# Optimization experiments

Hardware: AMD Instinct MI355X
Metric: run time of the kernel (lower is better)

Reference implementation:

```python
import jax, jax.numpy as jnp
import numpy as np

N, E, XD = 100000, 300000, 32
H, C = 4, 64          # heads, per-head out channels
D = H * C             # 256, node feature width
L = 3                 # num_message_passing
EPS = 1e-5
NEG_SLOPE = 0.2


def setup_inputs() -> dict:
    key = jax.random.key(0)
    ks = jax.random.split(key, 16)
    s = 0.05
    return {
        "x": jax.random.normal(ks[0], (N, XD), jnp.float32),
        "edge_index": jax.random.randint(ks[1], (2, E), 0, N, jnp.int32),
        "edge_type": jax.random.randint(ks[2], (E,), 0, 3, jnp.int32),
        "edge_feat": jax.random.uniform(ks[3], (E,), jnp.float32),
        # pre-encoder Linear(x_dim -> D)
        "W0": jax.random.normal(ks[4], (XD, D), jnp.float32) * s,
        "b0": jnp.zeros((D,), jnp.float32),
        # per-layer GATv2 params, stacked over L layers
        "Wl": jax.random.normal(ks[5], (L, D, D), jnp.float32) * s,
        "bl": jnp.zeros((L, D), jnp.float32),
        "Wr": jax.random.normal(ks[6], (L, D, D), jnp.float32) * s,
        "br": jnp.zeros((L, D), jnp.float32),
        "We": jax.random.normal(ks[7], (L, 4, D), jnp.float32) * s,  # lin_edge (no bias)
        "att": jax.random.normal(ks[8], (L, H, C), jnp.float32) * s,
        "bo": jnp.zeros((L, D), jnp.float32),
        # graph-mode LayerNorm (single module, reused every layer)
        "gamma": jnp.ones((D,), jnp.float32),
        "beta": jnp.zeros((D,), jnp.float32),
    }


def _graph_layernorm(h, gamma, beta):
    # PyG LayerNorm(mode='graph'): normalize over ALL nodes and features of the graph
    mu = jnp.mean(h)
    hc = h - mu
    var = jnp.mean(hc * hc)
    return hc * jax.lax.rsqrt(var + EPS) * gamma + beta


def _gatv2_layer(h, src, dst, eattr, Wl, bl, Wr, br, We, att, bo):
    xl = (h @ Wl + bl).reshape(N, H, C)
    xr = (h @ Wr + br).reshape(N, H, C)
    ea = (eattr @ We).reshape(E, H, C)
    e = jax.nn.leaky_relu(xl[src] + xr[dst] + ea, NEG_SLOPE)   # [E,H,C]
    alpha = jnp.einsum('ehc,hc->eh', e, att)                    # [E,H]
    amax = jax.ops.segment_max(alpha, dst, num_segments=N)     # [N,H]
    ex = jnp.exp(alpha - amax[dst])
    denom = jax.ops.segment_sum(ex, dst, num_segments=N)       # [N,H]
    a = ex / denom[dst]                                         # softmax per dst node
    msg = xl[src] * a[:, :, None]                               # [E,H,C]
    out = jax.ops.segment_sum(msg, dst, num_segments=N)        # [N,H,C]
    return out.reshape(N, D) + bo


def reference(x, edge_index, edge_type, edge_feat,
              W0, b0, Wl, bl, Wr, br, We, att, bo, gamma, beta):
    # edge feature construction: one-hot(type over 3) ++ scalar feature (== torch cat/where path)
    eattr = jnp.concatenate(
        [jax.nn.one_hot(edge_type, 3, dtype=x.dtype), edge_feat[:, None]], axis=-1)  # [E,4]
    src, dst = edge_index[0], edge_index[1]   # messages flow src -> dst
    h = jax.nn.relu(x @ W0 + b0)              # pre_enc (dropout = identity in eval)
    for i in range(L):
        g = _gatv2_layer(h, src, dst, eattr, Wl[i], bl[i], Wr[i], br[i], We[i], att[i], bo[i])
        h = _graph_layernorm(jax.nn.relu(g), gamma, beta)
    return h
```

## Files before the change

### kernel.cpp

```cpp
#include <hip/hip_runtime.h>
#include <hip/hip_bf16.h>

#define NN 100000
#define EE 300000
#define DD 256
#define HH 4
#define CC 64
#define LL 3
#define SCAN_CHUNK 1024

#define MPAD 100096

typedef __attribute__((ext_vector_type(8))) short bh8;
typedef __attribute__((ext_vector_type(4))) float f32x4;

__device__ inline float bf2f(unsigned short u) {
    union { float f; unsigned int i; } c; c.i = ((unsigned int)u) << 16; return c.f;
}
__device__ inline unsigned short f2bf(float x) {
    __hip_bfloat16 b = __float2bfloat16(x);
    return *reinterpret_cast<unsigned short*>(&b);
}


__global__ __launch_bounds__(256) void k_count(const int* __restrict__ dst, int* __restrict__ deg, int E_) {
    int e = blockIdx.x * 256 + threadIdx.x;
    if (e < E_) atomicAdd(&deg[dst[e]], 1);
}

__global__ __launch_bounds__(256) void k_scan1(const int* __restrict__ deg, int* __restrict__ bsum, int n) {
    int b = blockIdx.x;
    int base = b * SCAN_CHUNK;
    int t = threadIdx.x;
    int s = 0;
    for (int i = t; i < SCAN_CHUNK; i += 256) {
        int idx = base + i;
        if (idx < n) s += deg[idx];
    }
    __shared__ int sdata[256];
    sdata[t] = s;
    __syncthreads();
    for (int off = 128; off > 0; off >>= 1) {
        if (t < off) sdata[t] += sdata[t + off];
        __syncthreads();
    }
    if (t == 0) bsum[b] = sdata[0];
}

__global__ void k_scan2(const int* __restrict__ bsum, int* __restrict__ boff, int nb,
                        int* __restrict__ offsets, int n) {
    if (threadIdx.x == 0 && blockIdx.x == 0) {
        int run = 0;
        for (int i = 0; i < nb; i++) { boff[i] = run; run += bsum[i]; }
        offsets[n] = run;
    }
}

__global__ __launch_bounds__(256) void k_scan3(const int* __restrict__ deg, const int* __restrict__ boff,
                                               int* __restrict__ offsets, int n) {
    int b = blockIdx.x, t = threadIdx.x;
    int base = b * SCAN_CHUNK;
    int i0 = base + t * 4;
    int v[4]; int sum = 0;
    #pragma unroll
    for (int j = 0; j < 4; j++) {
        int idx = i0 + j;
        v[j] = (idx < n) ? deg[idx] : 0;
        sum += v[j];
    }
    __shared__ int sdata[256];
    sdata[t] = sum;
    __syncthreads();
    for (int off = 1; off < 256; off <<= 1) {
        int x = (t >= off) ? sdata[t - off] : 0;
        __syncthreads();
        sdata[t] += x;
        __syncthreads();
    }
    int excl = (t == 0) ? 0 : sdata[t - 1];
    int run = boff[b] + excl;
    #pragma unroll
    for (int j = 0; j < 4; j++) {
        int idx = i0 + j;
        if (idx < n) offsets[idx] = run;
        run += v[j];
    }
}

__global__ __launch_bounds__(256) void k_fill(const int* __restrict__ src, const int* __restrict__ dst,
                                              const int* __restrict__ ety, const float* __restrict__ efe,
                                              const int* __restrict__ offsets, int* __restrict__ cursor,
                                              int* __restrict__ csr_src, float* __restrict__ csr_feat, int E_) {
    int e = blockIdx.x * 256 + threadIdx.x;
    if (e < E_) {
        int d = dst[e];
        int pos = offsets[d] + atomicAdd(&cursor[d], 1);
        csr_src[pos] = src[e] | (ety[e] << 24);
        csr_feat[pos] = efe[e];
    }
}

__global__ __launch_bounds__(256) void k_cvtw(const float* __restrict__ Wl, const float* __restrict__ Wr,
                                              unsigned short* __restrict__ Wct) {
    int mat = blockIdx.z;
    int layer = mat >> 1, which = mat & 1;
    const float* src = (which ? Wr : Wl) + (size_t)layer * DD * DD;
    unsigned short* dst = Wct + (size_t)layer * 512 * DD + (size_t)which * DD * DD;
    int k0 = blockIdx.x * 64, n0 = blockIdx.y * 64;
    __shared__ float tile[64][65];
    int tx = threadIdx.x & 63, ty = threadIdx.x >> 6;
    #pragma unroll
    for (int i = 0; i < 16; i++) {
        int r = i * 4 + ty;
        tile[r][tx] = src[(size_t)(k0 + r) * DD + n0 + tx];
    }
    __syncthreads();
    #pragma unroll
    for (int i = 0; i < 16; i++) {
        int r = i * 4 + ty;
        dst[(size_t)(n0 + r) * DD + k0 + tx] = f2bf(tile[tx][r]);
    }
}

__global__ __launch_bounds__(256) void k_bias(const float* __restrict__ bl, const float* __restrict__ br,
                                              float* __restrict__ bc) {
    int i = blockIdx.x * 256 + threadIdx.x;
    if (i < LL * 512) {
        int l = i >> 9, j = i & 511;
        bc[i] = (j < 256) ? bl[l * DD + j] : br[l * DD + j - 256];
    }
}

__global__ __launch_bounds__(256) void k_preenc(const float* __restrict__ x, const float* __restrict__ W0,
                                                const float* __restrict__ b0, unsigned short* __restrict__ act) {
    __shared__ float xs[8][32];
    int t = threadIdx.x;
    int nb = blockIdx.x * 8;
    {
        int m = t >> 5, k = t & 31;
        xs[m][k] = x[(size_t)(nb + m) * 32 + k];
    }
    __syncthreads();
    float acc[8];
    float b = b0[t];
    #pragma unroll
    for (int m = 0; m < 8; m++) acc[m] = b;
    for (int k = 0; k < 32; k++) {
        float w = W0[k * DD + t];
        #pragma unroll
        for (int m = 0; m < 8; m++) acc[m] += xs[m][k] * w;
    }
    #pragma unroll
    for (int m = 0; m < 8; m++) {
        act[(size_t)(nb + m) * DD + t] = f2bf(fmaxf(acc[m], 0.f));
    }
}

__global__ __launch_bounds__(256, 3) void k_gemm(const unsigned short* __restrict__ act,
                                                 const unsigned short* __restrict__ Wct,
                                                 const float* __restrict__ bc,
                                                 unsigned short* __restrict__ xlr) {
    __shared__ short As[128][136];
    int t = threadIdx.x;
    int lane = t & 63;
    int w = t >> 6;
    int wm = w >> 1, wn = w & 1;
    size_t rowBase = (size_t)blockIdx.x * 128;
    int n0 = blockIdx.y * 128;
    int rsel = lane & 15, kq = lane >> 4;

    const unsigned short* Bw = Wct + (size_t)(n0 + wn * 64) * DD;

    f32x4 acc[4][4];
    #pragma unroll
    for (int i = 0; i < 4; i++)
        #pragma unroll
        for (int j = 0; j < 4; j++)
            acc[i][j] = (f32x4){0.f, 0.f, 0.f, 0.f};

    #pragma unroll
    for (int j = 0; j < 8; j++) {
        int idx = t + j * 256;
        int row = idx >> 4, c = idx & 15;
        *(bh8*)&As[row][c * 8] = *(const bh8*)(act + (rowBase + row) * DD + c * 8);
    }

    bh8 bcur[4], bnxt[4];
    #pragma unroll
    for (int ni = 0; ni < 4; ni++)
        bcur[ni] = *(const bh8*)(Bw + (size_t)(ni * 16 + rsel) * DD + kq * 8);

    __syncthreads();

    #pragma unroll
    for (int s = 0; s < 8; ++s) {
        if (s == 4) {
            __syncthreads();
            #pragma unroll
            for (int j = 0; j < 8; j++) {
                int idx = t + j * 256;
                int row = idx >> 4, c = idx & 15;
                *(bh8*)&As[row][c * 8] = *(const bh8*)(act + (rowBase + row) * DD + 128 + c * 8);
            }
            __syncthreads();
        }
        if (s < 7) {
            int s2 = s + 1;
            int kb2 = (s2 >> 2) * 128 + (s2 & 3) * 32 + kq * 8;
            #pragma unroll
            for (int ni = 0; ni < 4; ni++)
                bnxt[ni] = *(const bh8*)(Bw + (size_t)(ni * 16 + rsel) * DD + kb2);
        }
        int ksel = (s & 3) * 32 + kq * 8;
        bh8 af[4];
        #pragma unroll
        for (int mi = 0; mi < 4; mi++)
            af[mi] = *(const bh8*)&As[wm * 64 + mi * 16 + rsel][ksel];
        #pragma unroll
        for (int mi = 0; mi < 4; mi++)
            #pragma unroll
            for (int ni = 0; ni < 4; ni++)
                acc[mi][ni] = __builtin_amdgcn_mfma_f32_16x16x32_bf16(af[mi], bcur[ni], acc[mi][ni], 0, 0, 0);
        #pragma unroll
        for (int ni = 0; ni < 4; ni++) bcur[ni] = bnxt[ni];
    }

    __syncthreads();
    short* stage = &As[0][0];
    #pragma unroll
    for (int ni = 0; ni < 4; ni++) {
        int col = wn * 64 + ni * 16 + rsel;
        float bias = bc[n0 + col];
        #pragma unroll
        for (int mi = 0; mi < 4; mi++) {
            int r0 = wm * 64 + mi * 16 + kq * 4;
            #pragma unroll
            for (int j = 0; j < 4; j++)
                stage[(r0 + j) * 136 + col] = (short)f2bf(acc[mi][ni][j] + bias);
        }
    }
    __syncthreads();
    #pragma unroll
    for (int j = 0; j < 8; j++) {
        int idx = t + j * 256;
        int row = idx >> 4, c = idx & 15;
        size_t grow = rowBase + row;
        if (grow < NN)
            *(bh8*)(xlr + grow * 512 + n0 + c * 8) = *(const bh8*)&stage[row * 136 + c * 8];
    }
}

__global__ __launch_bounds__(256) void k_aggregate(const unsigned short* __restrict__ xlr,
                                                   const int* __restrict__ offsets,
                                                   const int* __restrict__ csr_src, const float* __restrict__ csr_feat,
                                                   const float* __restrict__ We, const float* __restrict__ att,
                                                   const float* __restrict__ bo,
                                                   unsigned short* __restrict__ act, float2* __restrict__ partial) {
    int lane = threadIdx.x & 63;
    int n = blockIdx.x * 4 + (threadIdx.x >> 6);
    int c0 = lane * 4;

    float4 attv = *(const float4*)(att + c0);
    float4 we3 = *(const float4*)(We + 3 * DD + c0);
    float4 w0v = *(const float4*)(We + 0 * DD + c0);
    float4 w1v = *(const float4*)(We + 1 * DD + c0);
    float4 w2v = *(const float4*)(We + 2 * DD + c0);

    uint2 xrr = *(const uint2*)(xlr + (size_t)n * 512 + 256 + c0);
    float xr0 = bf2f((unsigned short)(xrr.x & 0xffff));
    float xr1 = bf2f((unsigned short)(xrr.x >> 16));
    float xr2 = bf2f((unsigned short)(xrr.y & 0xffff));
    float xr3 = bf2f((unsigned short)(xrr.y >> 16));

    float b00 = xr0 + w0v.x, b01 = xr1 + w0v.y, b02 = xr2 + w0v.z, b03 = xr3 + w0v.w;
    float b10 = xr0 + w1v.x, b11 = xr1 + w1v.y, b12 = xr2 + w1v.z, b13 = xr3 + w1v.w;
    float b20 = xr0 + w2v.x, b21 = xr1 + w2v.y, b22 = xr2 + w2v.z, b23 = xr3 + w2v.w;

    int start = offsets[n], end = offsets[n + 1];
    float s = 0.f, a0 = 0.f, a1 = 0.f, a2 = 0.f, a3 = 0.f;
    int i = start;
    for (; i + 2 <= end; i += 2) {
        int pA = csr_src[i];     float fA = csr_feat[i];
        int pB = csr_src[i + 1]; float fB = csr_feat[i + 1];
        uint2 xvA = *(const uint2*)(xlr + (size_t)(pA & 0xFFFFF) * 512 + c0);
        uint2 xvB = *(const uint2*)(xlr + (size_t)(pB & 0xFFFFF) * 512 + c0);
        int tyA = pA >> 24, tyB = pB >> 24;
        float xA0 = bf2f((unsigned short)(xvA.x & 0xffff));
        float xA1 = bf2f((unsigned short)(xvA.x >> 16));
        float xA2 = bf2f((unsigned short)(xvA.y & 0xffff));
        float xA3 = bf2f((unsigned short)(xvA.y >> 16));
        float xB0 = bf2f((unsigned short)(xvB.x & 0xffff));
        float xB1 = bf2f((unsigned short)(xvB.x >> 16));
        float xB2 = bf2f((unsigned short)(xvB.y & 0xffff));
        float xB3 = bf2f((unsigned short)(xvB.y >> 16));
        float sA0 = (tyA == 0) ? b00 : (tyA == 1) ? b10 : b20;
        float sA1 = (tyA == 0) ? b01 : (tyA == 1) ? b11 : b21;
        float sA2 = (tyA == 0) ? b02 : (tyA == 1) ? b12 : b22;
        float sA3 = (tyA == 0) ? b03 : (tyA == 1) ? b13 : b23;
        float sB0 = (tyB == 0) ? b00 : (tyB == 1) ? b10 : b20;
        float sB1 = (tyB == 0) ? b01 : (tyB == 1) ? b11 : b21;
        float sB2 = (tyB == 0) ? b02 : (tyB == 1) ? b12 : b22;
        float sB3 = (tyB == 0) ? b03 : (tyB == 1) ? b13 : b23;
        float eA0 = xA0 + fmaf(fA, we3.x, sA0); eA0 = fmaxf(eA0, 0.2f * eA0);
        float eA1 = xA1 + fmaf(fA, we3.y, sA1); eA1 = fmaxf(eA1, 0.2f * eA1);
        float eA2 = xA2 + fmaf(fA, we3.z, sA2); eA2 = fmaxf(eA2, 0.2f * eA2);
        float eA3 = xA3 + fmaf(fA, we3.w, sA3); eA3 = fmaxf(eA3, 0.2f * eA3);
        float eB0 = xB0 + fmaf(fB, we3.x, sB0); eB0 = fmaxf(eB0, 0.2f * eB0);
        float eB1 = xB1 + fmaf(fB, we3.y, sB1); eB1 = fmaxf(eB1, 0.2f * eB1);
        float eB2 = xB2 + fmaf(fB, we3.z, sB2); eB2 = fmaxf(eB2, 0.2f * eB2);
        float eB3 = xB3 + fmaf(fB, we3.w, sB3); eB3 = fmaxf(eB3, 0.2f * eB3);
        float dA = attv.x * eA0 + attv.y * eA1 + attv.z * eA2 + attv.w * eA3;
        float dB = attv.x * eB0 + attv.y * eB1 + attv.z * eB2 + attv.w * eB3;
        dA += __shfl_xor(dA, 1, 64);  dB += __shfl_xor(dB, 1, 64);
        dA += __shfl_xor(dA, 2, 64);  dB += __shfl_xor(dB, 2, 64);
        dA += __shfl_xor(dA, 4, 64);  dB += __shfl_xor(dB, 4, 64);
        dA += __shfl_xor(dA, 8, 64);  dB += __shfl_xor(dB, 8, 64);
        float pa = __expf(fminf(fmaxf(dA, -60.f), 60.f));
        float pb = __expf(fminf(fmaxf(dB, -60.f), 60.f));
        s += pa + pb;
        a0 = fmaf(pa, xA0, fmaf(pb, xB0, a0));
        a1 = fmaf(pa, xA1, fmaf(pb, xB1, a1));
        a2 = fmaf(pa, xA2, fmaf(pb, xB2, a2));
        a3 = fmaf(pa, xA3, fmaf(pb, xB3, a3));
    }
    if (i < end) {
        int pA = csr_src[i]; float fA = csr_feat[i];
        uint2 xvA = *(const uint2*)(xlr + (size_t)(pA & 0xFFFFF) * 512 + c0);
        int tyA = pA >> 24;
        float xA0 = bf2f((unsigned short)(xvA.x & 0xffff));
        float xA1 = bf2f((unsigned short)(xvA.x >> 16));
        float xA2 = bf2f((unsigned short)(xvA.y & 0xffff));
        float xA3 = bf2f((unsigned short)(xvA.y >> 16));
        float sA0 = (tyA == 0) ? b00 : (tyA == 1) ? b10 : b20;
        float sA1 = (tyA == 0) ? b01 : (tyA == 1) ? b11 : b21;
        float sA2 = (tyA == 0) ? b02 : (tyA == 1) ? b12 : b22;
        float sA3 = (tyA == 0) ? b03 : (tyA == 1) ? b13 : b23;
        float eA0 = xA0 + fmaf(fA, we3.x, sA0); eA0 = fmaxf(eA0, 0.2f * eA0);
        float eA1 = xA1 + fmaf(fA, we3.y, sA1); eA1 = fmaxf(eA1, 0.2f * eA1);
        float eA2 = xA2 + fmaf(fA, we3.z, sA2); eA2 = fmaxf(eA2, 0.2f * eA2);
        float eA3 = xA3 + fmaf(fA, we3.w, sA3); eA3 = fmaxf(eA3, 0.2f * eA3);
        float dA = attv.x * eA0 + attv.y * eA1 + attv.z * eA2 + attv.w * eA3;
        dA += __shfl_xor(dA, 1, 64);
        dA += __shfl_xor(dA, 2, 64);
        dA += __shfl_xor(dA, 4, 64);
        dA += __shfl_xor(dA, 8, 64);
        float pa = __expf(fminf(fmaxf(dA, -60.f), 60.f));
        s += pa;
        a0 = fmaf(pa, xA0, a0);
        a1 = fmaf(pa, xA1, a1);
        a2 = fmaf(pa, xA2, a2);
        a3 = fmaf(pa, xA3, a3);
    }
    float inv = (end > start) ? __builtin_amdgcn_rcpf(s) : 0.f;
    float4 bov = *(const float4*)(bo + c0);
    float o0 = fmaxf(fmaf(a0, inv, bov.x), 0.f);
    float o1 = fmaxf(fmaf(a1, inv, bov.y), 0.f);
    float o2 = fmaxf(fmaf(a2, inv, bov.z), 0.f);
    float o3 = fmaxf(fmaf(a3, inv, bov.w), 0.f);
    uint2 pk;
    pk.x = (unsigned int)f2bf(o0) | ((unsigned int)f2bf(o1) << 16);
    pk.y = (unsigned int)f2bf(o2) | ((unsigned int)f2bf(o3) << 16);
    *(uint2*)(act + (size_t)n * DD + c0) = pk;

    float v1 = o0 + o1 + o2 + o3;
    float v2 = o0 * o0 + o1 * o1 + o2 * o2 + o3 * o3;
    #pragma unroll
    for (int off = 32; off > 0; off >>= 1) {
        v1 += __shfl_xor(v1, off, 64);
        v2 += __shfl_xor(v2, off, 64);
    }
    if (lane == 0) partial[n] = make_float2(v1, v2);
}

__global__ __launch_bounds__(256) void k_lnreduce(const float2* __restrict__ partial,
                                                  double2* __restrict__ partial2) {
    int b = blockIdx.x, t = threadIdx.x;
    double s1 = 0.0, s2 = 0.0;
    for (int i = b * 256 + t; i < NN; i += 64 * 256) {
        float2 p = partial[i];
        s1 += p.x; s2 += p.y;
    }
    __shared__ double d1[256], d2[256];
    d1[t] = s1; d2[t] = s2;
    __syncthreads();
    for (int off = 128; off > 0; off >>= 1) {
        if (t < off) { d1[t] += d1[t + off]; d2[t] += d2[t + off]; }
        __syncthreads();
    }
    if (t == 0) partial2[b] = (double2){d1[0], d2[0]};
}

__global__ __launch_bounds__(256) void k_stats(const double2* __restrict__ partial2,
                                               const float* __restrict__ gamma, const float* __restrict__ beta,
                                               float* __restrict__ sc, float* __restrict__ vsh) {
    __shared__ double d1[64], d2[64];
    int t = threadIdx.x;
    if (t < 64) { double2 p = partial2[t]; d1[t] = p.x; d2[t] = p.y; }
    __syncthreads();
    for (int off = 32; off > 0; off >>= 1) {
        if (t < off) { d1[t] += d1[t + off]; d2[t] += d2[t + off]; }
        __syncthreads();
    }
    const double M = (double)NN * DD;
    double mu = d1[0] / M;
    double var = d2[0] / M - mu * mu;
    float rs = rsqrtf((float)(var + 1e-5));
    float scv = rs * gamma[t];
    sc[t] = scv;
    vsh[t] = beta[t] - (float)mu * scv;
}

__global__ __launch_bounds__(256) void k_foldw(const unsigned short* __restrict__ Wct,
                                               const float* __restrict__ bcL,
                                               const float* __restrict__ sc, const float* __restrict__ vsh,
                                               unsigned short* __restrict__ Wct2, float* __restrict__ bc2) {
    int row = (blockIdx.x << 2) + (threadIdx.x >> 6);
    int lane = threadIdx.x & 63;
    int k0 = lane * 4;
    uint2 raw = *(const uint2*)(Wct + (size_t)row * DD + k0);
    float w0 = bf2f((unsigned short)(raw.x & 0xffff));
    float w1 = bf2f((unsigned short)(raw.x >> 16));
    float w2 = bf2f((unsigned short)(raw.y & 0xffff));
    float w3 = bf2f((unsigned short)(raw.y >> 16));
    float4 scv = *(const float4*)(sc + k0);
    float4 vv  = *(const float4*)(vsh + k0);
    uint2 pk;
    pk.x = (unsigned int)f2bf(w0 * scv.x) | ((unsigned int)f2bf(w1 * scv.y) << 16);
    pk.y = (unsigned int)f2bf(w2 * scv.z) | ((unsigned int)f2bf(w3 * scv.w) << 16);
    *(uint2*)(Wct2 + (size_t)row * DD + k0) = pk;
    float d = w0 * vv.x + w1 * vv.y + w2 * vv.z + w3 * vv.w;
    #pragma unroll
    for (int off = 32; off > 0; off >>= 1) d += __shfl_xor(d, off, 64);
    if (lane == 0) bc2[row] = bcL[row] + d;
}

__global__ __launch_bounds__(256) void k_final(const unsigned short* __restrict__ act,
                                               const float* __restrict__ sc, const float* __restrict__ vsh,
                                               float* __restrict__ h) {
    size_t i = ((size_t)blockIdx.x * 256 + threadIdx.x) * 4;
    uint2 raw = *(const uint2*)(act + i);
    int ch = (int)(i & (DD - 1));
    float4 scv = *(const float4*)(sc + ch);
    float4 vv  = *(const float4*)(vsh + ch);
    float4 o;
    o.x = fmaf(bf2f((unsigned short)(raw.x & 0xffff)), scv.x, vv.x);
    o.y = fmaf(bf2f((unsigned short)(raw.x >> 16)),    scv.y, vv.y);
    o.z = fmaf(bf2f((unsigned short)(raw.y & 0xffff)), scv.z, vv.z);
    o.w = fmaf(bf2f((unsigned short)(raw.y >> 16)),    scv.w, vv.w);
    *reinterpret_cast<float4*>(h + i) = o;
}


extern "C" void kernel_launch(void* const* d_in, const int* in_sizes, int n_in,
                              void* d_out, int out_size, void* d_ws, size_t ws_size,
                              hipStream_t stream) {
    const float* x    = (const float*)d_in[0];
    const int*   ei   = (const int*)d_in[1];
    const int*   ety  = (const int*)d_in[2];
    const float* efe  = (const float*)d_in[3];
    const float* W0   = (const float*)d_in[4];
    const float* b0   = (const float*)d_in[5];
    const float* Wl   = (const float*)d_in[6];
    const float* bl   = (const float*)d_in[7];
    const float* Wr   = (const float*)d_in[8];
    const float* br   = (const float*)d_in[9];
    const float* We   = (const float*)d_in[10];
    const float* att  = (const float*)d_in[11];
    const float* bo   = (const float*)d_in[12];
    const float* gamma= (const float*)d_in[13];
    const float* beta = (const float*)d_in[14];
    float* h = (float*)d_out;

    char* base = (char*)d_ws;
    size_t off = 0;
    auto carve = [&](size_t bytes) -> void* {
        void* p = base + off;
        off += (bytes + 255) & ~(size_t)255;
        return p;
    };
    unsigned short* act  = (unsigned short*)carve((size_t)MPAD * DD * 2);
    unsigned short* xlr  = (unsigned short*)carve((size_t)NN * 512 * 2);
    unsigned short* Wct  = (unsigned short*)carve((size_t)LL * 512 * DD * 2);
    unsigned short* Wct2 = (unsigned short*)carve((size_t)512 * DD * 2);
    float* bc            = (float*)carve((size_t)LL * 512 * 4);
    float* bc2           = (float*)carve((size_t)512 * 4);
    float* sc            = (float*)carve((size_t)DD * 4);
    float* vsh           = (float*)carve((size_t)DD * 4);
    int*   deg      = (int*)carve((size_t)NN * 4);
    int*   offsets  = (int*)carve((size_t)(NN + 1) * 4);
    int*   bsum     = (int*)carve(1024);
    int*   boff     = (int*)carve(1024);
    int*   csr_src  = (int*)carve((size_t)EE * 4);
    float* csr_feat = (float*)carve((size_t)EE * 4);
    float2* partial = (float2*)carve((size_t)NN * 8);
    double2* partial2 = (double2*)carve((size_t)64 * 16);

    const int NB = (NN + SCAN_CHUNK - 1) / SCAN_CHUNK;

    hipMemsetAsync(deg, 0, (size_t)NN * 4, stream);
    k_count<<<(EE + 255) / 256, 256, 0, stream>>>(ei + EE, deg, EE);
    k_scan1<<<NB, 256, 0, stream>>>(deg, bsum, NN);
    k_scan2<<<1, 64, 0, stream>>>(bsum, boff, NB, offsets, NN);
    k_scan3<<<NB, 256, 0, stream>>>(deg, boff, offsets, NN);
    hipMemsetAsync(deg, 0, (size_t)NN * 4, stream);
    k_fill<<<(EE + 255) / 256, 256, 0, stream>>>(ei, ei + EE, ety, efe, offsets, deg,
                                                 csr_src, csr_feat, EE);

    k_cvtw<<<dim3(4, 4, 6), 256, 0, stream>>>(Wl, Wr, Wct);
    k_bias<<<6, 256, 0, stream>>>(bl, br, bc);

    k_preenc<<<NN / 8, 256, 0, stream>>>(x, W0, b0, act);

    for (int l = 0; l < LL; l++) {
        const unsigned short* Wg = (l == 0) ? Wct : Wct2;
        const float* bg = (l == 0) ? bc : bc2;
        k_gemm<<<dim3(MPAD / 128, 4), 256, 0, stream>>>(act, Wg, bg, xlr);
        k_aggregate<<<NN / 4, 256, 0, stream>>>(xlr, offsets, csr_src, csr_feat,
                                                We + (size_t)l * 4 * DD, att + (size_t)l * HH * CC,
                                                bo + (size_t)l * DD, act, partial);
        k_lnreduce<<<64, 256, 0, stream>>>(partial, partial2);
        k_stats<<<1, 256, 0, stream>>>(partial2, gamma, beta, sc, vsh);
        if (l < LL - 1)
            k_foldw<<<128, 256, 0, stream>>>(Wct + (size_t)(l + 1) * 512 * DD, bc + (size_t)(l + 1) * 512,
                                             sc, vsh, Wct2, bc2);
    }
    k_final<<<(NN * DD / 4) / 256, 256, 0, stream>>>(act, sc, vsh, h);
}
```

Measured before the change: 542.0 us.

## Retile GEMM to 64-row blocks covering all 512 output columns

The GEMM block now loads a 64-row activation tile with the full K=256 into LDS once, and uses 8 waves that each compute 64 output columns, so one block covers all 512 columns. Previously a 2D grid used 128x128 tiles, which reloaded each activation row four times and refilled LDS midway through K. The output is staged in two halves through LDS. This removes redundant activation reads, but each wave now streams its own weight slice, and occupancy changes with the 512-thread blocks and the larger LDS footprint.

```diff
diff --git a/kernel.cpp b/kernel.cpp
--- a/kernel.cpp
+++ b/kernel.cpp
@@ -156,20 +156,25 @@
     }
 }
 
-__global__ __launch_bounds__(256, 3) void k_gemm(const unsigned short* __restrict__ act,
-                                                 const unsigned short* __restrict__ Wct,
-                                                 const float* __restrict__ bc,
-                                                 unsigned short* __restrict__ xlr) {
-    __shared__ short As[128][136];
+__global__ __launch_bounds__(512) void k_gemm(const unsigned short* __restrict__ act,
+                                              const unsigned short* __restrict__ Wct,
+                                              const float* __restrict__ bc,
+                                              unsigned short* __restrict__ xlr) {
+    __shared__ short lds[16896];
     int t = threadIdx.x;
     int lane = t & 63;
     int w = t >> 6;
-    int wm = w >> 1, wn = w & 1;
-    size_t rowBase = (size_t)blockIdx.x * 128;
-    int n0 = blockIdx.y * 128;
+    size_t rowBase = (size_t)blockIdx.x * 64;
     int rsel = lane & 15, kq = lane >> 4;
 
-    const unsigned short* Bw = Wct + (size_t)(n0 + wn * 64) * DD;
+    #pragma unroll
+    for (int j = 0; j < 4; j++) {
+        int idx = t + j * 512;
+        int row = idx >> 5, c = idx & 31;
+        *(bh8*)&lds[row * 260 + c * 8] = *(const bh8*)(act + (rowBase + row) * DD + c * 8);
+    }
+
+    const unsigned short* Bw = Wct + (size_t)(w * 64) * DD;
 
     f32x4 acc[4][4];
     #pragma unroll
@@ -178,13 +183,6 @@
         for (int j = 0; j < 4; j++)
             acc[i][j] = (f32x4){0.f, 0.f, 0.f, 0.f};
 
-    #pragma unroll
-    for (int j = 0; j < 8; j++) {
-        int idx = t + j * 256;
-        int row = idx >> 4, c = idx & 15;
-        *(bh8*)&As[row][c * 8] = *(const bh8*)(act + (rowBase + row) * DD + c * 8);
-    }
-
     bh8 bcur[4], bnxt[4];
     #pragma unroll
     for (int ni = 0; ni < 4; ni++)
@@ -193,29 +191,17 @@
     __syncthreads();
 
     #pragma unroll
-    for (int s = 0; s < 8; ++s) {
-        if (s == 4) {
-            __syncthreads();
-            #pragma unroll
-            for (int j = 0; j < 8; j++) {
-                int idx = t + j * 256;
-                int row = idx >> 4, c = idx & 15;
-                *(bh8*)&As[row][c * 8] = *(const bh8*)(act + (rowBase + row) * DD + 128 + c * 8);
-            }
-            __syncthreads();
-        }
-        if (s < 7) {
-            int s2 = s + 1;
-            int kb2 = (s2 >> 2) * 128 + (s2 & 3) * 32 + kq * 8;
+    for (int ks = 0; ks < 8; ++ks) {
+        if (ks < 7) {
+            int ko = (ks + 1) * 32 + kq * 8;
             #pragma unroll
             for (int ni = 0; ni < 4; ni++)
-                bnxt[ni] = *(const bh8*)(Bw + (size_t)(ni * 16 + rsel) * DD + kb2);
+                bnxt[ni] = *(const bh8*)(Bw + (size_t)(ni * 16 + rsel) * DD + ko);
         }
-        int ksel = (s & 3) * 32 + kq * 8;
         bh8 af[4];
         #pragma unroll
         for (int mi = 0; mi < 4; mi++)
-            af[mi] = *(const bh8*)&As[wm * 64 + mi * 16 + rsel][ksel];
+            af[mi] = *(const bh8*)&lds[(mi * 16 + rsel) * 260 + ks * 32 + kq * 8];
         #pragma unroll
         for (int mi = 0; mi < 4; mi++)
             #pragma unroll
@@ -225,28 +211,33 @@
         for (int ni = 0; ni < 4; ni++) bcur[ni] = bnxt[ni];
     }
 
-    __syncthreads();
-    short* stage = &As[0][0];
-    #pragma unroll
-    for (int ni = 0; ni < 4; ni++) {
-        int col = wn * 64 + ni * 16 + rsel;
-        float bias = bc[n0 + col];
+    #pragma unroll
+    for (int h = 0; h < 2; ++h) {
+        __syncthreads();
+        if ((w >> 2) == h) {
+            int wl = w & 3;
+            #pragma unroll
+            for (int ni = 0; ni < 4; ni++) {
+                int col = wl * 64 + ni * 16 + rsel;
+                float bias = bc[h * 256 + col];
+                #pragma unroll
+                for (int mi = 0; mi < 4; mi++) {
+                    int r0 = mi * 16 + kq * 4;
+                    #pragma unroll
+                    for (int j = 0; j < 4; j++)
+                        lds[(r0 + j) * 264 + col] = (short)f2bf(acc[mi][ni][j] + bias);
+                }
+            }
+        }
+        __syncthreads();
         #pragma unroll
-        for (int mi = 0; mi < 4; mi++) {
-            int r0 = wm * 64 + mi * 16 + kq * 4;
-            #pragma unroll
-            for (int j = 0; j < 4; j++)
-                stage[(r0 + j) * 136 + col] = (short)f2bf(acc[mi][ni][j] + bias);
+        for (int j = 0; j < 4; ++j) {
+            int idx = t + j * 512;
+            int row = idx >> 5, c16 = idx & 31;
+            size_t grow = rowBase + row;
+            if (grow < NN)
+                *(bh8*)(xlr + grow * 512 + h * 256 + c16 * 8) = *(const bh8*)&lds[row * 264 + c16 * 8];
         }
-    }
-    __syncthreads();
-    #pragma unroll
-    for (int j = 0; j < 8; j++) {
-        int idx = t + j * 256;
-        int row = idx >> 4, c = idx & 15;
-        size_t grow = rowBase + row;
-        if (grow < NN)
-            *(bh8*)(xlr + grow * 512 + n0 + c * 8) = *(const bh8*)&stage[row * 136 + c * 8];
     }
 }
 
@@ -514,7 +505,7 @@
     for (int l = 0; l < LL; l++) {
         const unsigned short* Wg = (l == 0) ? Wct : Wct2;
         const float* bg = (l == 0) ? bc : bc2;
-        k_gemm<<<dim3(MPAD / 128, 4), 256, 0, stream>>>(act, Wg, bg, xlr);
+        k_gemm<<<MPAD / 64, 512, 0, stream>>>(act, Wg, bg, xlr);
         k_aggregate<<<NN / 4, 256, 0, stream>>>(xlr, offsets, csr_src, csr_feat,
                                                 We + (size_t)l * 4 * DD, att + (size_t)l * HH * CC,
                                                 bo + (size_t)l * DD, act, partial);
```

New measurement: 567.3 us (median of 3 runs). 1.05x slower.
